# Performance work log

Measured on AMD Instinct MI355X. Metric: run time of the kernel, lower is better.

Reference implementation:

```python
import jax, jax.numpy as jnp
import numpy as np
import math

N, DM, DK, DV, KWIN = 500, 2048, 2048, 2048, 10

def _xavier(key, shape):
    fan_out, fan_in = shape[0], shape[1]
    limit = math.sqrt(6.0 / (fan_in + fan_out))
    return jax.random.uniform(key, (shape[0], shape[1]), jnp.float32, -limit, limit)

def setup_inputs() -> dict:
    key = jax.random.key(0)
    ks = jax.random.split(key, 7)
    X = jax.random.normal(ks[0], (N, DM), jnp.float32)
    mask = jax.random.randint(ks[1], (N, N), 0, 2, jnp.int32)
    # torch Linear weight is (out, in); store transposed so fwd is X @ W
    Wq = _xavier(ks[2], (DK, DM)).T  # [DM, DK]
    Wk = _xavier(ks[3], (DK, DM)).T
    Wv = _xavier(ks[4], (DV, DM)).T
    Wo = _xavier(ks[5], (DM, DV)).T  # [DV, DM]
    wk = _xavier(ks[6], (2 * KWIN + 1, DM))  # relative-position embedding table
    return {"X": X, "mask": mask, "Wq": Wq, "Wk": Wk, "Wv": Wv, "Wo": Wo, "wk": wk}

def reference(X, mask, Wq, Wk, Wv, Wo, wk):
    n = X.shape[0]
    scale = 1.0 / math.sqrt(DK)
    Q = X @ Wq            # [n, dk]
    K = X @ Wk            # [n, dk]
    V = X @ Wv            # [n, dv]
    Qs = Q * scale
    S = Qs @ K.T          # [n, n] content scores
    # relative-position bias: Sr[i,j] = Qs[i] . wk[clip(j-i,-k,k)+k]
    # (Shaw-style gather; identical math to wk[table] matmul, no [n,n,dm] intermediate)
    idx = jnp.clip(jnp.arange(n)[None, :] - jnp.arange(n)[:, None], -KWIN, KWIN) + KWIN  # [n, n]
    QR = Qs @ wk.T                                   # [n, 2k+1]
    Sr = jnp.take_along_axis(QR, idx, axis=1)        # [n, n]
    S = S + Sr
    S = jnp.where(mask == 0, jnp.float32(-1e9), S)
    A = jax.nn.softmax(S, axis=-1)                   # dropout_rate=0 -> identity
    Y = (A @ V) @ Wo                                 # [n, dm]
    return (Y, A)
```

## Files before the change

kernel.cpp:

```cpp
#include <hip/hip_runtime.h>
#include <hip/hip_bf16.h>


#define N_TOK 500
#define MP 512
#define DM 2048
#define KWIN_ 10
#define NREL 21

typedef __hip_bfloat16 bf16;
typedef __attribute__((ext_vector_type(8))) short short8;
typedef __attribute__((ext_vector_type(4))) float floatx4;

#define NQK 2097152L
#define NVT 1048576L
#define NS 262144L
#define NY 1048576L

__device__ inline float bfj(const short8& v, int j) {
  return __bfloat162float(((const bf16*)&v)[j]);
}

__global__ __launch_bounds__(256) void prep(
    const float* __restrict__ Wq, const float* __restrict__ Wk,
    const float* __restrict__ Wv, const float* __restrict__ Wo,
    const float* __restrict__ X, const float* __restrict__ wk,
    bf16* __restrict__ WqkT, bf16* __restrict__ WvT, bf16* __restrict__ WoT,
    bf16* __restrict__ Xb, bf16* __restrict__ wkb) {
  int z = blockIdx.z;
  int tid = threadIdx.x;
  if (z == 4) {
    int row = blockIdx.y * 32 + blockIdx.x;
    int c0 = tid * 8;
    bf16 v[8];
    if (row < MP) {
      if (row < N_TOK) {
        const float* p = X + (long)row * DM + c0;
#pragma unroll
        for (int j = 0; j < 8; ++j) v[j] = __float2bfloat16(p[j]);
      } else {
#pragma unroll
        for (int j = 0; j < 8; ++j) v[j] = __float2bfloat16(0.f);
      }
      *(short8*)(Xb + (long)row * DM + c0) = *(short8*)v;
    } else if (row < MP + NREL) {
      int r = row - MP;
      const float* p = wk + (long)r * DM + c0;
#pragma unroll
      for (int j = 0; j < 8; ++j) v[j] = __float2bfloat16(p[j]);
      *(short8*)(wkb + (long)r * DM + c0) = *(short8*)v;
    }
    return;
  }
  const float* W = (z == 0) ? Wq : (z == 1) ? Wk : (z == 2) ? Wv : Wo;
  bf16* Out = (z == 0) ? WqkT
            : (z == 1) ? (WqkT + (long)DM * DM)
            : (z == 2) ? WvT : WoT;
  __shared__ float t[64][68];
  int k0 = blockIdx.y * 64, n0 = blockIdx.x * 64;
  int rr = tid >> 4, cc = (tid & 15) * 4;
  int gsw = cc >> 2;
#pragma unroll
  for (int p = 0; p < 4; ++p) {
    int r = rr + 16 * p;
    float4 v = *(const float4*)(W + (long)(k0 + r) * DM + n0 + cc);
    *(float4*)&t[r][(gsw ^ (r & 3)) * 4] = v;
  }
  __syncthreads();
#pragma unroll
  for (int s0 = 0; s0 < 2; ++s0) {
    int s = tid + s0 * 256;
    int n = s >> 3, c = s & 7;
    bf16 v[8];
#pragma unroll
    for (int j = 0; j < 8; ++j) {
      int rowt = c * 8 + j;
      int col = ((n >> 2) ^ (rowt & 3)) * 4 + (n & 3);
      v[j] = __float2bfloat16(t[rowt][col]);
    }
    *(short8*)(Out + (long)(n0 + n) * DM + k0 + c * 8) = *(short8*)v;
  }
}

template <int OUT>
__device__ __forceinline__ void gemm_core(
    const bf16* __restrict__ A, int lda, const bf16* __restrict__ B, int ldb,
    float* __restrict__ Cf, bf16* __restrict__ Cb, int ldc, int kStart,
    int kLen, int row0, int col0) {
  __shared__ __align__(16) bf16 As[128][32];
  __shared__ __align__(16) bf16 Bs[128][32];
  int tid = threadIdx.x;
  int lane = tid & 63, w = tid >> 6;
  int wr = (w & 1) * 64, wc = (w >> 1) * 64;
  int l16 = lane & 15, l4 = lane >> 4;
  int r1 = tid >> 2, c1 = (tid & 3) * 8;
  const bf16* Ab = A + (long)row0 * lda + kStart;
  const bf16* Bb = B + (long)col0 * ldb + kStart;
  const bf16* a1p = Ab + (long)r1 * lda + c1;
  const bf16* a2p = Ab + (long)(r1 + 64) * lda + c1;
  const bf16* b1p = Bb + (long)r1 * ldb + c1;
  const bf16* b2p = Bb + (long)(r1 + 64) * ldb + c1;
  floatx4 acc[4][4] = {};
  short8 pa0 = *(const short8*)a1p, pa1 = *(const short8*)a2p;
  short8 pb0 = *(const short8*)b1p, pb1 = *(const short8*)b2p;
  for (int k0 = 0; k0 < kLen; k0 += 32) {
    if (k0) __syncthreads();
    *(short8*)&As[r1][c1] = pa0;
    *(short8*)&As[r1 + 64][c1] = pa1;
    *(short8*)&Bs[r1][c1] = pb0;
    *(short8*)&Bs[r1 + 64][c1] = pb1;
    __syncthreads();
    int kn = k0 + 32;
    if (kn < kLen) {
      pa0 = *(const short8*)(a1p + kn);
      pa1 = *(const short8*)(a2p + kn);
      pb0 = *(const short8*)(b1p + kn);
      pb1 = *(const short8*)(b2p + kn);
    }
    short8 af[4], bg[4];
#pragma unroll
    for (int g = 0; g < 4; ++g)
      af[g] = *(short8*)&As[wr + g * 16 + l16][l4 * 8];
#pragma unroll
    for (int g = 0; g < 4; ++g)
      bg[g] = *(short8*)&Bs[wc + g * 16 + l16][l4 * 8];
#pragma unroll
    for (int g = 0; g < 4; ++g)
#pragma unroll
      for (int h = 0; h < 4; ++h)
        acc[g][h] =
            __builtin_amdgcn_mfma_f32_16x16x32_bf16(af[g], bg[h], acc[g][h], 0, 0, 0);
  }
#pragma unroll
  for (int g = 0; g < 4; ++g)
#pragma unroll
    for (int h = 0; h < 4; ++h)
#pragma unroll
      for (int i = 0; i < 4; ++i) {
        long r = row0 + wr + g * 16 + l4 * 4 + i;
        long c = col0 + wc + h * 16 + l16;
        if (OUT == 0)
          Cf[r * ldc + c] = acc[g][h][i];
        else
          Cb[r * ldc + c] = __float2bfloat16(acc[g][h][i]);
      }
}

__global__ __launch_bounds__(256, 2) void gemm_qkvt(
    const bf16* __restrict__ Xb, const bf16* __restrict__ WqkT,
    const bf16* __restrict__ WvT, float* __restrict__ QKp,
    float* __restrict__ Vtp) {
  int id = blockIdx.x;
  if (id < 256) {
    int z = id >> 7, t = id & 127;
    int col0 = (t & 31) * 128, row0 = (t >> 5) * 128;
    gemm_core<0>(Xb, DM, WqkT, DM, QKp + (long)z * NQK, nullptr, 4096,
                 z * 1024, 1024, row0, col0);
  } else {
    int id2 = id - 256;
    int z = id2 >> 6, t = id2 & 63;
    int col0 = (t & 3) * 128, row0 = (t >> 2) * 128;
    gemm_core<0>(WvT, DM, Xb, DM, Vtp + (long)z * NVT, nullptr, MP, z * 1024,
                 1024, row0, col0);
  }
}

template <int OUT>
__global__ __launch_bounds__(256, 2) void gemm_k(
    const bf16* __restrict__ A, int lda, const bf16* __restrict__ B, int ldb,
    float* __restrict__ Cf, bf16* __restrict__ Cb, int ldc, int sliceK,
    long cstride) {
  float* cf = (OUT == 0) ? Cf + (long)blockIdx.z * cstride : nullptr;
  gemm_core<OUT>(A, lda, B, ldb, cf, Cb, ldc, blockIdx.z * sliceK, sliceK,
                 blockIdx.y * 128, blockIdx.x * 128);
}

__global__ __launch_bounds__(256) void reduce_qkvt(
    const float* __restrict__ QKp, const float* __restrict__ Vtp,
    bf16* __restrict__ QKbf, bf16* __restrict__ Vtb) {
  long e = ((long)blockIdx.x * 256 + threadIdx.x) * 8;
  const float* p0;
  long stride;
  bf16* out;
  long eo;
  if (e < NQK) {
    p0 = QKp + e; stride = NQK; out = QKbf; eo = e;
  } else {
    eo = e - NQK; p0 = Vtp + eo; stride = NVT; out = Vtb;
  }
  float4 a0 = *(const float4*)p0, a1 = *(const float4*)(p0 + 4);
  float4 b0 = *(const float4*)(p0 + stride), b1 = *(const float4*)(p0 + stride + 4);
  bf16 v[8];
  v[0] = __float2bfloat16(a0.x + b0.x); v[1] = __float2bfloat16(a0.y + b0.y);
  v[2] = __float2bfloat16(a0.z + b0.z); v[3] = __float2bfloat16(a0.w + b0.w);
  v[4] = __float2bfloat16(a1.x + b1.x); v[5] = __float2bfloat16(a1.y + b1.y);
  v[6] = __float2bfloat16(a1.z + b1.z); v[7] = __float2bfloat16(a1.w + b1.w);
  *(short8*)(out + eo) = *(short8*)v;
}

__global__ __launch_bounds__(256) void reduce_y(const float* __restrict__ Yp,
                                                float* __restrict__ Yout) {
  long e = (long)blockIdx.x * 2048 + threadIdx.x * 8;
  float4 a0 = *(const float4*)(Yp + e), a1 = *(const float4*)(Yp + e + 4);
  float4 b0 = *(const float4*)(Yp + NY + e), b1 = *(const float4*)(Yp + NY + e + 4);
  float4 o0 = {a0.x + b0.x, a0.y + b0.y, a0.z + b0.z, a0.w + b0.w};
  float4 o1 = {a1.x + b1.x, a1.y + b1.y, a1.z + b1.z, a1.w + b1.w};
  *(float4*)(Yout + e) = o0;
  *(float4*)(Yout + e + 4) = o1;
}

__global__ __launch_bounds__(256) void softmax_qr(
    const float* __restrict__ Sp, const bf16* __restrict__ QKbf,
    const bf16* __restrict__ wkb, const int* __restrict__ mask,
    float* __restrict__ Aout, bf16* __restrict__ Abf) {
  int i = blockIdx.x;
  int tid = threadIdx.x;
  if (i >= N_TOK) {
    Abf[(long)i * MP + tid] = __float2bfloat16(0.f);
    Abf[(long)i * MP + tid + 256] = __float2bfloat16(0.f);
    return;
  }
  int lane = tid & 63, w = tid >> 6;
  __shared__ float sQR[24];
  __shared__ float red[4];
  short8 q[4];
#pragma unroll
  for (int s = 0; s < 4; ++s)
    q[s] = *(const short8*)(QKbf + (long)i * 4096 + s * 512 + lane * 8);
  for (int r = w; r < NREL; r += 4) {
    float p = 0.f;
#pragma unroll
    for (int s = 0; s < 4; ++s) {
      short8 wv = *(const short8*)(wkb + (long)r * DM + s * 512 + lane * 8);
#pragma unroll
      for (int j = 0; j < 8; ++j) p += bfj(q[s], j) * bfj(wv, j);
    }
#pragma unroll
    for (int o = 32; o > 0; o >>= 1) p += __shfl_down(p, o);
    if (lane == 0) sQR[r] = p;
  }
  __syncthreads();
  const float scale = 0.022097086912079608f;
  float v0, v1 = -1e30f;
  int j0 = tid, j1 = tid + 256;
  {
    float s = Sp[(long)i * MP + j0] + Sp[NS + (long)i * MP + j0] +
              Sp[2 * NS + (long)i * MP + j0] + Sp[3 * NS + (long)i * MP + j0];
    int rel = j0 - i;
    rel = rel < -KWIN_ ? -KWIN_ : (rel > KWIN_ ? KWIN_ : rel);
    s = scale * (s + sQR[rel + KWIN_]);
    if (mask[(long)i * N_TOK + j0] == 0) s = -1e9f;
    v0 = s;
  }
  if (j1 < N_TOK) {
    float s = Sp[(long)i * MP + j1] + Sp[NS + (long)i * MP + j1] +
              Sp[2 * NS + (long)i * MP + j1] + Sp[3 * NS + (long)i * MP + j1];
    int rel = j1 - i;
    rel = rel < -KWIN_ ? -KWIN_ : (rel > KWIN_ ? KWIN_ : rel);
    s = scale * (s + sQR[rel + KWIN_]);
    if (mask[(long)i * N_TOK + j1] == 0) s = -1e9f;
    v1 = s;
  }
  float mx = fmaxf(v0, v1);
#pragma unroll
  for (int o = 32; o > 0; o >>= 1) mx = fmaxf(mx, __shfl_down(mx, o));
  if (lane == 0) red[w] = mx;
  __syncthreads();
  if (tid == 0) red[0] = fmaxf(fmaxf(red[0], red[1]), fmaxf(red[2], red[3]));
  __syncthreads();
  mx = red[0];
  __syncthreads();
  float e0 = expf(v0 - mx);
  float e1 = (j1 < N_TOK) ? expf(v1 - mx) : 0.f;
  float sum = e0 + e1;
#pragma unroll
  for (int o = 32; o > 0; o >>= 1) sum += __shfl_down(sum, o);
  if (lane == 0) red[w] = sum;
  __syncthreads();
  if (tid == 0) red[0] = red[0] + red[1] + red[2] + red[3];
  __syncthreads();
  float inv = 1.f / red[0];
  float a0 = e0 * inv, a1 = e1 * inv;
  Aout[(long)i * N_TOK + j0] = a0;
  if (j1 < N_TOK) Aout[(long)i * N_TOK + j1] = a1;
  Abf[(long)i * MP + j0] = __float2bfloat16(a0);
  Abf[(long)i * MP + j1] = __float2bfloat16(a1);
}

extern "C" void kernel_launch(void* const* d_in, const int* in_sizes, int n_in,
                              void* d_out, int out_size, void* d_ws,
                              size_t ws_size, hipStream_t stream) {
  const float* X = (const float*)d_in[0];
  const int* mask = (const int*)d_in[1];
  const float* Wq = (const float*)d_in[2];
  const float* Wk = (const float*)d_in[3];
  const float* Wv = (const float*)d_in[4];
  const float* Wo = (const float*)d_in[5];
  const float* wk = (const float*)d_in[6];

  float* Yout = (float*)d_out;
  float* Aout = Yout + (long)N_TOK * DM;

  const long MB = 1 << 20;
  char* p = (char*)d_ws;
  bf16* Xb = (bf16*)p;
  bf16* WqkT = (bf16*)(p + 2 * MB);
  bf16* WvT = (bf16*)(p + 18 * MB);
  bf16* WoT = (bf16*)(p + 26 * MB);
  bf16* wkb = (bf16*)(p + 34 * MB);
  float* QKp = (float*)(p + 35 * MB);
  float* Vtp = (float*)(p + 51 * MB);
  bf16* QKbf = (bf16*)(p + 59 * MB);
  bf16* Vtb = (bf16*)(p + 63 * MB);
  float* Sp = (float*)(p + 65 * MB);
  bf16* Abf = (bf16*)(p + 69 * MB);
  bf16* AVbf = (bf16*)(p + 70 * MB);
  float* Yp = (float*)(p + 72 * MB);

  dim3 b256(256);

  prep<<<dim3(32, 32, 5), b256, 0, stream>>>(Wq, Wk, Wv, Wo, X, wk, WqkT, WvT,
                                             WoT, Xb, wkb);
  gemm_qkvt<<<dim3(384), b256, 0, stream>>>(Xb, WqkT, WvT, QKp, Vtp);
  reduce_qkvt<<<dim3(1536), b256, 0, stream>>>(QKp, Vtp, QKbf, Vtb);
  gemm_k<0><<<dim3(4, 4, 4), b256, 0, stream>>>(QKbf, 4096, QKbf + 2048, 4096,
                                                Sp, nullptr, MP, 512, NS);
  softmax_qr<<<dim3(MP), b256, 0, stream>>>(Sp, QKbf, wkb, mask, Aout, Abf);
  gemm_k<1><<<dim3(16, 4, 1), b256, 0, stream>>>(Abf, MP, Vtb, MP, nullptr,
                                                 AVbf, DM, MP, 0);
  gemm_k<0><<<dim3(16, 4, 2), b256, 0, stream>>>(AVbf, DM, WoT, DM, Yp,
                                                 nullptr, DM, 1024, NY);
  reduce_y<<<dim3(N_TOK), b256, 0, stream>>>(Yp, Yout);
}
```

Before: 193.7 us.

## Use direct-to-LDS double-buffered GEMM loads and drop split-K reductions

The GEMM core now issues global_load_lds directly into a double-buffered shared tile, overlapping the next k-slice load with the MFMA work on the current one. A 64-row tile variant is added so the GEMMs that used split-K can run full-K with more blocks. This lets the fp32 partial buffers and both reduction kernels be removed, and the QKV and output GEMMs now write bf16 or the final fp32 output directly. The trade-off is fewer blocks per GEMM for the QKV pass, plus hand-written waitcnt accounting that must match the number of loads in flight.

```diff
diff --git a/kernel.cpp b/kernel.cpp
--- a/kernel.cpp
+++ b/kernel.cpp
@@ -12,13 +12,16 @@
 typedef __attribute__((ext_vector_type(8))) short short8;
 typedef __attribute__((ext_vector_type(4))) float floatx4;
 
-#define NQK 2097152L
-#define NVT 1048576L
 #define NS 262144L
-#define NY 1048576L
 
 __device__ inline float bfj(const short8& v, int j) {
   return __bfloat162float(((const bf16*)&v)[j]);
+}
+
+__device__ __forceinline__ void gload16(const bf16* g, bf16* l) {
+  __builtin_amdgcn_global_load_lds(
+      (const __attribute__((address_space(1))) void*)g,
+      (__attribute__((address_space(3))) void*)l, 16, 0, 0);
 }
 
 __global__ __launch_bounds__(256) void prep(
@@ -82,131 +85,115 @@
   }
 }
 
-template <int OUT>
+template <int BM, int OUT>
 __device__ __forceinline__ void gemm_core(
-    const bf16* __restrict__ A, int lda, const bf16* __restrict__ B, int ldb,
-    float* __restrict__ Cf, bf16* __restrict__ Cb, int ldc, int kStart,
-    int kLen, int row0, int col0) {
-  __shared__ __align__(16) bf16 As[128][32];
-  __shared__ __align__(16) bf16 Bs[128][32];
+    bf16 (*sm)[256][32], const bf16* __restrict__ A, int lda,
+    const bf16* __restrict__ B, int ldb, float* __restrict__ Cf,
+    bf16* __restrict__ Cb, int ldc, int kStart, int kLen, int row0, int col0,
+    int mLim) {
+  constexpr int GM = (BM == 128) ? 4 : 2;
   int tid = threadIdx.x;
   int lane = tid & 63, w = tid >> 6;
-  int wr = (w & 1) * 64, wc = (w >> 1) * 64;
   int l16 = lane & 15, l4 = lane >> 4;
-  int r1 = tid >> 2, c1 = (tid & 3) * 8;
+  int lrow = lane >> 2, lcol = (lane & 3) * 8;
+  int wr = (w & 1) * (16 * GM), wc = (w >> 1) * 64;
   const bf16* Ab = A + (long)row0 * lda + kStart;
   const bf16* Bb = B + (long)col0 * ldb + kStart;
-  const bf16* a1p = Ab + (long)r1 * lda + c1;
-  const bf16* a2p = Ab + (long)(r1 + 64) * lda + c1;
-  const bf16* b1p = Bb + (long)r1 * ldb + c1;
-  const bf16* b2p = Bb + (long)(r1 + 64) * ldb + c1;
-  floatx4 acc[4][4] = {};
-  short8 pa0 = *(const short8*)a1p, pa1 = *(const short8*)a2p;
-  short8 pb0 = *(const short8*)b1p, pb1 = *(const short8*)b2p;
+  const int arow0 = (BM == 128) ? 32 * w : 16 * w;
+  const bf16* aSrc0 = Ab + (long)(arow0 + lrow) * lda + lcol;
+  const bf16* aSrc1 = Ab + (long)(arow0 + 16 + lrow) * lda + lcol;
+  const bf16* bSrc0 = Bb + (long)(32 * w + lrow) * ldb + lcol;
+  const bf16* bSrc1 = Bb + (long)(32 * w + 16 + lrow) * ldb + lcol;
+
+  floatx4 acc[GM][4] = {};
+
+#define STAGE(buf, kk)                                          \
+  do {                                                          \
+    gload16(aSrc0 + (kk), &sm[buf][arow0][0]);                  \
+    if (BM == 128) gload16(aSrc1 + (kk), &sm[buf][arow0 + 16][0]); \
+    gload16(bSrc0 + (kk), &sm[buf][128 + 32 * w][0]);           \
+    gload16(bSrc1 + (kk), &sm[buf][128 + 32 * w + 16][0]);      \
+  } while (0)
+
+  STAGE(0, 0);
+  int cur = 0;
   for (int k0 = 0; k0 < kLen; k0 += 32) {
-    if (k0) __syncthreads();
-    *(short8*)&As[r1][c1] = pa0;
-    *(short8*)&As[r1 + 64][c1] = pa1;
-    *(short8*)&Bs[r1][c1] = pb0;
-    *(short8*)&Bs[r1 + 64][c1] = pb1;
-    __syncthreads();
     int kn = k0 + 32;
     if (kn < kLen) {
-      pa0 = *(const short8*)(a1p + kn);
-      pa1 = *(const short8*)(a2p + kn);
-      pb0 = *(const short8*)(b1p + kn);
-      pb1 = *(const short8*)(b2p + kn);
+      STAGE(cur ^ 1, kn);
+      if (BM == 128)
+        asm volatile("s_waitcnt vmcnt(4)" ::: "memory");
+      else
+        asm volatile("s_waitcnt vmcnt(3)" ::: "memory");
+    } else {
+      asm volatile("s_waitcnt vmcnt(0)" ::: "memory");
     }
-    short8 af[4], bg[4];
-#pragma unroll
-    for (int g = 0; g < 4; ++g)
-      af[g] = *(short8*)&As[wr + g * 16 + l16][l4 * 8];
-#pragma unroll
-    for (int g = 0; g < 4; ++g)
-      bg[g] = *(short8*)&Bs[wc + g * 16 + l16][l4 * 8];
-#pragma unroll
-    for (int g = 0; g < 4; ++g)
+    __builtin_amdgcn_s_barrier();
+    __builtin_amdgcn_sched_barrier(0);
+    short8 af[GM], bg[4];
+#pragma unroll
+    for (int g = 0; g < GM; ++g)
+      af[g] = *(const short8*)&sm[cur][wr + g * 16 + l16][l4 * 8];
+#pragma unroll
+    for (int h = 0; h < 4; ++h)
+      bg[h] = *(const short8*)&sm[cur][128 + wc + h * 16 + l16][l4 * 8];
+#pragma unroll
+    for (int g = 0; g < GM; ++g)
 #pragma unroll
       for (int h = 0; h < 4; ++h)
-        acc[g][h] =
-            __builtin_amdgcn_mfma_f32_16x16x32_bf16(af[g], bg[h], acc[g][h], 0, 0, 0);
-  }
-#pragma unroll
-  for (int g = 0; g < 4; ++g)
+        acc[g][h] = __builtin_amdgcn_mfma_f32_16x16x32_bf16(af[g], bg[h],
+                                                            acc[g][h], 0, 0, 0);
+    __builtin_amdgcn_sched_barrier(0);
+    asm volatile("s_waitcnt lgkmcnt(0)" ::: "memory");
+    __builtin_amdgcn_s_barrier();
+    cur ^= 1;
+  }
+#undef STAGE
+
+#pragma unroll
+  for (int g = 0; g < GM; ++g)
 #pragma unroll
     for (int h = 0; h < 4; ++h)
 #pragma unroll
       for (int i = 0; i < 4; ++i) {
         long r = row0 + wr + g * 16 + l4 * 4 + i;
         long c = col0 + wc + h * 16 + l16;
-        if (OUT == 0)
-          Cf[r * ldc + c] = acc[g][h][i];
-        else
-          Cb[r * ldc + c] = __float2bfloat16(acc[g][h][i]);
+        if (r < mLim) {
+          if (OUT == 0)
+            Cf[r * ldc + c] = acc[g][h][i];
+          else
+            Cb[r * ldc + c] = __float2bfloat16(acc[g][h][i]);
+        }
       }
 }
 
 __global__ __launch_bounds__(256, 2) void gemm_qkvt(
     const bf16* __restrict__ Xb, const bf16* __restrict__ WqkT,
-    const bf16* __restrict__ WvT, float* __restrict__ QKp,
-    float* __restrict__ Vtp) {
+    const bf16* __restrict__ WvT, bf16* __restrict__ QKbf,
+    bf16* __restrict__ Vtb) {
+  __shared__ __align__(16) bf16 sm[2][256][32];
   int id = blockIdx.x;
-  if (id < 256) {
-    int z = id >> 7, t = id & 127;
-    int col0 = (t & 31) * 128, row0 = (t >> 5) * 128;
-    gemm_core<0>(Xb, DM, WqkT, DM, QKp + (long)z * NQK, nullptr, 4096,
-                 z * 1024, 1024, row0, col0);
+  if (id < 128) {
+    int row0 = (id >> 5) * 128, col0 = (id & 31) * 128;
+    gemm_core<128, 1>(sm, Xb, DM, WqkT, DM, nullptr, QKbf, 4096, 0, DM, row0,
+                      col0, MP);
   } else {
-    int id2 = id - 256;
-    int z = id2 >> 6, t = id2 & 63;
-    int col0 = (t & 3) * 128, row0 = (t >> 2) * 128;
-    gemm_core<0>(WvT, DM, Xb, DM, Vtp + (long)z * NVT, nullptr, MP, z * 1024,
-                 1024, row0, col0);
-  }
-}
-
-template <int OUT>
+    int t = id - 128;
+    int row0 = (t >> 2) * 64, col0 = (t & 3) * 128;
+    gemm_core<64, 1>(sm, WvT, DM, Xb, DM, nullptr, Vtb, MP, 0, DM, row0, col0,
+                     DM);
+  }
+}
+
+template <int BM, int OUT>
 __global__ __launch_bounds__(256, 2) void gemm_k(
     const bf16* __restrict__ A, int lda, const bf16* __restrict__ B, int ldb,
     float* __restrict__ Cf, bf16* __restrict__ Cb, int ldc, int sliceK,
-    long cstride) {
+    long cstride, int mLim) {
+  __shared__ __align__(16) bf16 sm[2][256][32];
   float* cf = (OUT == 0) ? Cf + (long)blockIdx.z * cstride : nullptr;
-  gemm_core<OUT>(A, lda, B, ldb, cf, Cb, ldc, blockIdx.z * sliceK, sliceK,
-                 blockIdx.y * 128, blockIdx.x * 128);
-}
-
-__global__ __launch_bounds__(256) void reduce_qkvt(
-    const float* __restrict__ QKp, const float* __restrict__ Vtp,
-    bf16* __restrict__ QKbf, bf16* __restrict__ Vtb) {
-  long e = ((long)blockIdx.x * 256 + threadIdx.x) * 8;
-  const float* p0;
-  long stride;
-  bf16* out;
-  long eo;
-  if (e < NQK) {
-    p0 = QKp + e; stride = NQK; out = QKbf; eo = e;
-  } else {
-    eo = e - NQK; p0 = Vtp + eo; stride = NVT; out = Vtb;
-  }
-  float4 a0 = *(const float4*)p0, a1 = *(const float4*)(p0 + 4);
-  float4 b0 = *(const float4*)(p0 + stride), b1 = *(const float4*)(p0 + stride + 4);
-  bf16 v[8];
-  v[0] = __float2bfloat16(a0.x + b0.x); v[1] = __float2bfloat16(a0.y + b0.y);
-  v[2] = __float2bfloat16(a0.z + b0.z); v[3] = __float2bfloat16(a0.w + b0.w);
-  v[4] = __float2bfloat16(a1.x + b1.x); v[5] = __float2bfloat16(a1.y + b1.y);
-  v[6] = __float2bfloat16(a1.z + b1.z); v[7] = __float2bfloat16(a1.w + b1.w);
-  *(short8*)(out + eo) = *(short8*)v;
-}
-
-__global__ __launch_bounds__(256) void reduce_y(const float* __restrict__ Yp,
-                                                float* __restrict__ Yout) {
-  long e = (long)blockIdx.x * 2048 + threadIdx.x * 8;
-  float4 a0 = *(const float4*)(Yp + e), a1 = *(const float4*)(Yp + e + 4);
-  float4 b0 = *(const float4*)(Yp + NY + e), b1 = *(const float4*)(Yp + NY + e + 4);
-  float4 o0 = {a0.x + b0.x, a0.y + b0.y, a0.z + b0.z, a0.w + b0.w};
-  float4 o1 = {a1.x + b1.x, a1.y + b1.y, a1.z + b1.z, a1.w + b1.w};
-  *(float4*)(Yout + e) = o0;
-  *(float4*)(Yout + e + 4) = o1;
+  gemm_core<BM, OUT>(sm, A, lda, B, ldb, cf, Cb, ldc, blockIdx.z * sliceK,
+                     sliceK, blockIdx.y * BM, blockIdx.x * 128, mLim);
 }
 
 __global__ __launch_bounds__(256) void softmax_qr(
@@ -308,27 +295,22 @@
   bf16* WvT = (bf16*)(p + 18 * MB);
   bf16* WoT = (bf16*)(p + 26 * MB);
   bf16* wkb = (bf16*)(p + 34 * MB);
-  float* QKp = (float*)(p + 35 * MB);
-  float* Vtp = (float*)(p + 51 * MB);
-  bf16* QKbf = (bf16*)(p + 59 * MB);
-  bf16* Vtb = (bf16*)(p + 63 * MB);
-  float* Sp = (float*)(p + 65 * MB);
-  bf16* Abf = (bf16*)(p + 69 * MB);
-  bf16* AVbf = (bf16*)(p + 70 * MB);
-  float* Yp = (float*)(p + 72 * MB);
+  bf16* QKbf = (bf16*)(p + 35 * MB);
+  bf16* Vtb = (bf16*)(p + 39 * MB);
+  float* Sp = (float*)(p + 41 * MB);
+  bf16* Abf = (bf16*)(p + 45 * MB);
+  bf16* AVbf = (bf16*)(p + 46 * MB);
 
   dim3 b256(256);
 
   prep<<<dim3(32, 32, 5), b256, 0, stream>>>(Wq, Wk, Wv, Wo, X, wk, WqkT, WvT,
                                              WoT, Xb, wkb);
-  gemm_qkvt<<<dim3(384), b256, 0, stream>>>(Xb, WqkT, WvT, QKp, Vtp);
-  reduce_qkvt<<<dim3(1536), b256, 0, stream>>>(QKp, Vtp, QKbf, Vtb);
-  gemm_k<0><<<dim3(4, 4, 4), b256, 0, stream>>>(QKbf, 4096, QKbf + 2048, 4096,
-                                                Sp, nullptr, MP, 512, NS);
+  gemm_qkvt<<<dim3(256), b256, 0, stream>>>(Xb, WqkT, WvT, QKbf, Vtb);
+  gemm_k<64, 0><<<dim3(4, 8, 4), b256, 0, stream>>>(
+      QKbf, 4096, QKbf + 2048, 4096, Sp, nullptr, MP, 512, NS, MP);
   softmax_qr<<<dim3(MP), b256, 0, stream>>>(Sp, QKbf, wkb, mask, Aout, Abf);
-  gemm_k<1><<<dim3(16, 4, 1), b256, 0, stream>>>(Abf, MP, Vtb, MP, nullptr,
-                                                 AVbf, DM, MP, 0);
-  gemm_k<0><<<dim3(16, 4, 2), b256, 0, stream>>>(AVbf, DM, WoT, DM, Yp,
-                                                 nullptr, DM, 1024, NY);
-  reduce_y<<<dim3(N_TOK), b256, 0, stream>>>(Yp, Yout);
-}
+  gemm_k<64, 1><<<dim3(16, 8, 1), b256, 0, stream>>>(
+      Abf, MP, Vtb, MP, nullptr, AVbf, DM, MP, 0, MP);
+  gemm_k<64, 0><<<dim3(16, 8, 1), b256, 0, stream>>>(
+      AVbf, DM, WoT, DM, Yout, nullptr, DM, DM, 0, N_TOK);
+}
```

After: 189.4 us. -2.2%, faster.
